# Kernel optimization log

Measured on AMD Instinct MI355X. Metric: run time of the kernel, lower is better.

Reference implementation:

```python
import jax, jax.numpy as jnp
import numpy as np

B, N, C, H = 8, 1024, 768, 12
D = C // H  # head_dim = 64
SCALE = D ** -0.5


def setup_inputs() -> dict:
    key = jax.random.key(0)
    ks = jax.random.split(key, 5)
    s = lambda k, sh, fan: jax.random.normal(k, sh, jnp.float32) * (fan ** -0.5)
    return {
        "x": jax.random.normal(ks[0], (B, N, C), jnp.float32),
        "w_qkv": s(ks[1], (C, 3 * C), C),
        "b_qkv": jnp.zeros((3 * C,), jnp.float32),
        "w_l": s(ks[2], (H, H), H),
        "b_l": jnp.zeros((H,), jnp.float32),
        "w_w": s(ks[3], (H, H), H),
        "b_w": jnp.zeros((H,), jnp.float32),
        "w_proj": s(ks[4], (C, C), C),
        "b_proj": jnp.zeros((C,), jnp.float32),
    }


def reference(x, w_qkv, b_qkv, w_l, b_l, w_w, b_w, w_proj, b_proj):
    Bq, Nq, Cq = x.shape
    # qkv projection -> (3, B, H, N, D)
    qkv = (x @ w_qkv + b_qkv).reshape(Bq, Nq, 3, H, D).transpose(2, 0, 3, 1, 4)
    q, k, v = qkv[0] * SCALE, qkv[1], qkv[2]
    # raw scores [B, H, N, N]
    attn = jnp.einsum("bhnd,bhmd->bhnm", q, k)
    # pre-softmax talking-heads: mix across head axis (Dense over H)
    attn = jnp.einsum("bhnm,hg->bgnm", attn, w_l) + b_l[None, :, None, None]
    attn = jax.nn.softmax(attn, axis=-1)
    # post-softmax talking-heads
    attn = jnp.einsum("bhnm,hg->bgnm", attn, w_w) + b_w[None, :, None, None]
    # weighted values -> (B, N, C)
    out = jnp.einsum("bhnm,bhmd->bnhd", attn, v).reshape(Bq, Nq, Cq)
    return out @ w_proj + b_proj
```

## Files before the change

kernel.cpp:

```cpp
#include <hip/hip_runtime.h>

#define BB 8
#define NN 1024
#define CC 768
#define HH 12
#define DD 64

typedef unsigned short u16;
typedef unsigned int u32;
typedef __attribute__((ext_vector_type(8))) short s16x8;
typedef __attribute__((ext_vector_type(4))) short s16x4;
typedef __attribute__((ext_vector_type(4))) float f32x4;
typedef __attribute__((ext_vector_type(2))) u32 u32x2;
typedef __attribute__((ext_vector_type(4))) u32 u32x4;

__device__ __forceinline__ float bf2f(u16 u) {
  u32 x = ((u32)u) << 16;
  return __builtin_bit_cast(float, x);
}
__device__ __forceinline__ u16 f2bf(float f) {
  u32 x = __builtin_bit_cast(u32, f);
  x += 0x7fffu + ((x >> 16) & 1u);
  return (u16)(x >> 16);
}
__device__ __forceinline__ float hw_exp2(float x) { return __builtin_amdgcn_exp2f(x); }
__device__ __forceinline__ float hw_log2(float x) { return __builtin_amdgcn_logf(x); }
__device__ __forceinline__ s16x8 lds_read8(const u16* p) {
  u32x2 a = *(const u32x2*)p;
  u32x2 b = *(const u32x2*)(p + 4);
  u32x4 m = {a.x, a.y, b.x, b.y};
  return __builtin_bit_cast(s16x8, m);
}
__device__ __forceinline__ u32 packhl(float v) {
  u32 xv = __builtin_bit_cast(u32, v);
  float lo = v - __builtin_bit_cast(float, xv & 0xFFFF0000u);
  return (xv >> 16) | (__builtin_bit_cast(u32, lo) & 0xFFFF0000u);
}
__device__ __forceinline__ void gload_lds16(const u16* g, u16* l) {
  __builtin_amdgcn_global_load_lds(
      (const __attribute__((address_space(1))) u32*)g,
      (__attribute__((address_space(3))) u32*)l, 16, 0, 0);
}

__global__ __launch_bounds__(256) void convx_kernel(const float* __restrict__ in,
                                                    u16* __restrict__ out) {
  size_t i = ((size_t)blockIdx.x * 256 + threadIdx.x) * 8;
  f32x4 a = *(const f32x4*)(in + i);
  f32x4 b = *(const f32x4*)(in + i + 4);
  s16x8 r;
#pragma unroll
  for (int j = 0; j < 4; j++) { r[j] = (short)f2bf(a[j]); r[4 + j] = (short)f2bf(b[j]); }
  *(s16x8*)(out + i) = r;
}

__global__ __launch_bounds__(256) void transpose_kernel(const float* __restrict__ in,
                                                        u16* __restrict__ out,
                                                        int R, int C) {
  __shared__ float t[32][33];
  const int cl = threadIdx.x & 31, rq = threadIdx.x >> 5;
#pragma unroll
  for (int rr = 0; rr < 4; rr++) {
    int rl = rq * 4 + rr;
    t[rl][cl] = in[(size_t)(blockIdx.y * 32 + rl) * C + blockIdx.x * 32 + cl];
  }
  __syncthreads();
#pragma unroll
  for (int rr = 0; rr < 4; rr++) {
    int oc = rq * 4 + rr;
    out[(size_t)(blockIdx.x * 32 + oc) * R + blockIdx.y * 32 + cl] = f2bf(t[cl][oc]);
  }
}

__global__ __launch_bounds__(256) void qkv_gemm(
    const u16* __restrict__ A, const u16* __restrict__ Bt, const float* __restrict__ bias,
    u16* __restrict__ qo, u16* __restrict__ ko, u16* __restrict__ vo) {
  __shared__ __align__(16) u16 As[128 * 32];
  __shared__ __align__(16) u16 Bs[128 * 32];
  const int tid = threadIdx.x;
  const int w = tid >> 6, lane = tid & 63, l15 = lane & 15, l4 = lane >> 4;
  const int wm = w & 1, wn = w >> 1;
  const int m0 = blockIdx.x * 128, n0 = blockIdx.y * 128;
  const int grow = lane >> 2, gcol = (lane & 3) * 8;

  f32x4 acc[4][4];
#pragma unroll
  for (int a = 0; a < 4; a++)
#pragma unroll
    for (int bb = 0; bb < 4; bb++) acc[a][bb] = (f32x4){0.f, 0.f, 0.f, 0.f};

  for (int k0 = 0; k0 < CC; k0 += 32) {
    __syncthreads();
    const u16* ga = A + (size_t)(m0 + w * 32 + grow) * CC + k0 + gcol;
    const u16* gb = Bt + (size_t)(n0 + w * 32 + grow) * CC + k0 + gcol;
    gload_lds16(ga, &As[w * 1024]);
    gload_lds16(ga + (size_t)16 * CC, &As[w * 1024 + 512]);
    gload_lds16(gb, &Bs[w * 1024]);
    gload_lds16(gb + (size_t)16 * CC, &Bs[w * 1024 + 512]);
    __syncthreads();
    s16x8 af[4], bf[4];
#pragma unroll
    for (int a = 0; a < 4; a++) af[a] = *(const s16x8*)&As[(wm * 64 + a * 16 + l15) * 32 + l4 * 8];
#pragma unroll
    for (int bb = 0; bb < 4; bb++) bf[bb] = *(const s16x8*)&Bs[(wn * 64 + bb * 16 + l15) * 32 + l4 * 8];
#pragma unroll
    for (int a = 0; a < 4; a++)
#pragma unroll
      for (int bb = 0; bb < 4; bb++)
        acc[a][bb] = __builtin_amdgcn_mfma_f32_16x16x32_bf16(af[a], bf[bb], acc[a][bb], 0, 0, 0);
  }

  const int b = (m0 >> 10);
#pragma unroll
  for (int bb = 0; bb < 4; bb++) {
    int col = n0 + wn * 64 + bb * 16 + l15;
    int s = col / CC;
    int rem = col - s * CC;
    int h = rem >> 6, d = rem & 63;
    float bv = bias[col];
#pragma unroll
    for (int a = 0; a < 4; a++) {
      int row0 = m0 + wm * 64 + a * 16 + l4 * 4;
      int nt0 = row0 & (NN - 1);
      if (s == 2) {
        s16x4 pk;
#pragma unroll
        for (int r = 0; r < 4; r++) pk[r] = (short)f2bf(acc[a][bb][r] + bv);
        *(s16x4*)(vo + (((size_t)((b * HH + h) * DD + d)) << 10) + nt0) = pk;
      } else if (s == 0) {
#pragma unroll
        for (int r = 0; r < 4; r++)
          qo[(((size_t)((b * HH + h) * NN + nt0 + r)) << 6) + d] = f2bf((acc[a][bb][r] + bv) * 0.125f);
      } else {
#pragma unroll
        for (int r = 0; r < 4; r++)
          ko[(((size_t)((b * HH + h) * NN + nt0 + r)) << 6) + d] = f2bf(acc[a][bb][r] + bv);
      }
    }
  }
}

__global__ __launch_bounds__(256) void proj_gemm(
    const u16* __restrict__ A, const u16* __restrict__ Bt, const float* __restrict__ bias,
    float* __restrict__ out) {
  __shared__ __align__(16) u16 As[128 * 32];
  __shared__ __align__(16) u16 Bs[128 * 32];
  const int tid = threadIdx.x;
  const int w = tid >> 6, lane = tid & 63, l15 = lane & 15, l4 = lane >> 4;
  const int wm = w & 1, wn = w >> 1;
  const int m0 = blockIdx.x * 128, n0 = blockIdx.y * 128;
  const int grow = lane >> 2, gcol = (lane & 3) * 8;

  f32x4 acc[4][4];
#pragma unroll
  for (int a = 0; a < 4; a++)
#pragma unroll
    for (int bb = 0; bb < 4; bb++) acc[a][bb] = (f32x4){0.f, 0.f, 0.f, 0.f};

  for (int k0 = 0; k0 < CC; k0 += 32) {
    __syncthreads();
    const u16* ga = A + (size_t)(m0 + w * 32 + grow) * CC + k0 + gcol;
    const u16* gb = Bt + (size_t)(n0 + w * 32 + grow) * CC + k0 + gcol;
    gload_lds16(ga, &As[w * 1024]);
    gload_lds16(ga + (size_t)16 * CC, &As[w * 1024 + 512]);
    gload_lds16(gb, &Bs[w * 1024]);
    gload_lds16(gb + (size_t)16 * CC, &Bs[w * 1024 + 512]);
    __syncthreads();
    s16x8 af[4], bf[4];
#pragma unroll
    for (int a = 0; a < 4; a++) af[a] = *(const s16x8*)&As[(wm * 64 + a * 16 + l15) * 32 + l4 * 8];
#pragma unroll
    for (int bb = 0; bb < 4; bb++) bf[bb] = *(const s16x8*)&Bs[(wn * 64 + bb * 16 + l15) * 32 + l4 * 8];
#pragma unroll
    for (int a = 0; a < 4; a++)
#pragma unroll
      for (int bb = 0; bb < 4; bb++)
        acc[a][bb] = __builtin_amdgcn_mfma_f32_16x16x32_bf16(af[a], bf[bb], acc[a][bb], 0, 0, 0);
  }

#pragma unroll
  for (int bb = 0; bb < 4; bb++) {
    int col = n0 + wn * 64 + bb * 16 + l15;
    float bv = bias[col];
#pragma unroll
    for (int a = 0; a < 4; a++) {
      int row0 = m0 + wm * 64 + a * 16 + l4 * 4;
#pragma unroll
      for (int r = 0; r < 4; r++)
        out[(size_t)(row0 + r) * CC + col] = acc[a][bb][r] + bv;
    }
  }
}

#define SB_BYTES 28736
#define UT_OFF   SB_BYTES
#define UT_ELE   6912
#define LL2_OFF  (SB_BYTES + 27648)
#define SM_TOTAL (LL2_OFF + 1088)

__global__ __launch_bounds__(512, 4) void attn_kernel(
    const u16* __restrict__ qg, const u16* __restrict__ kg, const u16* __restrict__ vtg,
    const float* __restrict__ wlg, const float* __restrict__ blg,
    const float* __restrict__ wwg, const float* __restrict__ bwg,
    u16* __restrict__ aout) {
  __shared__ __align__(16) char smem[SM_TOTAL];
  u16* Sb = (u16*)smem;
  u16* Ut0 = (u16*)(smem + UT_OFF);
  float* lpart = (float*)(smem + UT_OFF);
  float* ll2 = (float*)(smem + LL2_OFF);

  const int b = blockIdx.x, i0 = blockIdx.y * 16;
  const int tid = threadIdx.x;
  const int w = tid >> 6, lane = tid & 63, l15 = lane & 15, l4 = lane >> 4;
  const float RLN2 = 1.44269504088896340736f;

  for (int j = tid; j < SB_BYTES / 4; j += 512) ((u32*)smem)[j] = 0;
  __syncthreads();

  s16x8 wlS, wlA1, wlA2, wwA1, wwA2;
#pragma unroll
  for (int j = 0; j < 8; j++) {
    int k = l4 * 8 + j;
    float v1 = (k < 12 && l15 < 12) ? wlg[k * 12 + l15] * RLN2 : 0.f;
    wlS[j] = (short)f2bf(v1);
    int h = k >> 1, pt = k & 1;
    float v2 = (h < 12 && l15 < 12) ? wlg[h * 12 + l15] * RLN2 : 0.f;
    u16 h2 = f2bf(v2); u16 lo2 = f2bf(v2 - bf2f(h2));
    wlA1[j] = (short)h2; wlA2[j] = (short)(pt ? 0 : lo2);
    float v3 = (h < 12 && l15 < 12) ? wwg[h * 12 + l15] : 0.f;
    u16 h3 = f2bf(v3); u16 lo3 = f2bf(v3 - bf2f(h3));
    wwA1[j] = (short)h3; wwA2[j] = (short)(pt ? 0 : lo3);
  }
  int gr[4]; float blv[4], bwv[4];
#pragma unroll
  for (int r = 0; r < 4; r++) {
    gr[r] = l4 * 4 + r;
    blv[r] = (gr[r] < 12) ? blg[gr[r]] * RLN2 : 0.f;
    bwv[r] = (gr[r] < 12) ? bwg[gr[r]] : 0.f;
  }

  int jh[3], jmb[3];
  s16x8 qf[3][2];
#pragma unroll
  for (int jt = 0; jt < 3; jt++) {
    int j = w * 3 + jt;
    jh[jt] = j % 12; jmb[jt] = j / 12;
    const u16* qp = qg + (((size_t)((b * HH + jh[jt]) * NN + i0 + l15)) << 6) + l4 * 8;
    qf[jt][0] = *(const s16x8*)qp;
    qf[jt][1] = *(const s16x8*)(qp + 32);
  }

  float la[4] = {0.f, 0.f, 0.f, 0.f};
  for (int mt = 0; mt < 32; mt++) {
    const int m0 = mt * 32;
#pragma unroll
    for (int jt = 0; jt < 3; jt++) {
      f32x4 c = (f32x4){0.f, 0.f, 0.f, 0.f};
      const u16* kp = kg + (((size_t)((b * HH + jh[jt]) * NN + m0 + jmb[jt] * 16 + l15)) << 6) + l4 * 8;
      c = __builtin_amdgcn_mfma_f32_16x16x32_bf16(*(const s16x8*)kp, qf[jt][0], c, 0, 0, 0);
      c = __builtin_amdgcn_mfma_f32_16x16x32_bf16(*(const s16x8*)(kp + 32), qf[jt][1], c, 0, 0, 0);
      int cb = (jmb[jt] * 16 + l4 * 4) * 16 + l15;
#pragma unroll
      for (int r = 0; r < 4; r++)
        Sb[(size_t)(cb + r * 16) * 20 + jh[jt]] = f2bf(c[r]);
    }
    __syncthreads();
#pragma unroll
    for (int tt = 0; tt < 4; tt++) {
      int t = w * 4 + tt;
      s16x8 bS = lds_read8(Sb + (size_t)(t * 16 + l15) * 20 + l4 * 8);
      f32x4 T = (f32x4){blv[0], blv[1], blv[2], blv[3]};
      T = __builtin_amdgcn_mfma_f32_16x16x32_bf16(wlS, bS, T, 0, 0, 0);
#pragma unroll
      for (int r = 0; r < 4; r++) la[r] += hw_exp2(T[r]);
    }
    __syncthreads();
  }

#pragma unroll
  for (int r = 0; r < 4; r++) lpart[w * 256 + gr[r] * 16 + l15] = la[r];
  __syncthreads();
  if (tid < 256) {
    float s = 0.f;
#pragma unroll
    for (int w2 = 0; w2 < 8; w2++) s += lpart[w2 * 256 + tid];
    ll2[(tid >> 4) * 17 + (tid & 15)] = hw_log2(s);
  }
  __syncthreads();
  float Tinit[4];
#pragma unroll
  for (int r = 0; r < 4; r++) Tinit[r] = blv[r] - ll2[gr[r] * 17 + l15];

  const int db = w >> 1, pvh = (w & 1) * 6;
  f32x4 O[6];
#pragma unroll
  for (int jp = 0; jp < 6; jp++) O[jp] = (f32x4){0.f, 0.f, 0.f, 0.f};

  for (int mt = 0; mt < 32; mt++) {
    const int m0 = mt * 32;
    u16* Utb = Ut0 + (mt & 1) * UT_ELE;
#pragma unroll
    for (int jt = 0; jt < 3; jt++) {
      f32x4 c = (f32x4){0.f, 0.f, 0.f, 0.f};
      const u16* kp = kg + (((size_t)((b * HH + jh[jt]) * NN + m0 + jmb[jt] * 16 + l15)) << 6) + l4 * 8;
      c = __builtin_amdgcn_mfma_f32_16x16x32_bf16(*(const s16x8*)kp, qf[jt][0], c, 0, 0, 0);
      c = __builtin_amdgcn_mfma_f32_16x16x32_bf16(*(const s16x8*)(kp + 32), qf[jt][1], c, 0, 0, 0);
      int cb = (jmb[jt] * 16 + l4 * 4) * 16 + l15;
#pragma unroll
      for (int r = 0; r < 4; r++)
        *(u32*)(Sb + (size_t)(cb + r * 16) * 28 + 2 * jh[jt]) = packhl(c[r]);
    }
    __syncthreads();
#pragma unroll
    for (int tt = 0; tt < 4; tt++) {
      int t = w * 4 + tt;
      s16x8 bS = lds_read8(Sb + (size_t)(t * 16 + l15) * 28 + l4 * 8);
      f32x4 T = (f32x4){Tinit[0], Tinit[1], Tinit[2], Tinit[3]};
      T = __builtin_amdgcn_mfma_f32_16x16x32_bf16(wlA1, bS, T, 0, 0, 0);
      T = __builtin_amdgcn_mfma_f32_16x16x32_bf16(wlA2, bS, T, 0, 0, 0);
      u32x4 pk;
#pragma unroll
      for (int r = 0; r < 4; r++) pk[r] = packhl(hw_exp2(T[r]));
      s16x8 bP = __builtin_bit_cast(s16x8, pk);
      f32x4 U = (f32x4){bwv[0], bwv[1], bwv[2], bwv[3]};
      U = __builtin_amdgcn_mfma_f32_16x16x32_bf16(wwA1, bP, U, 0, 0, 0);
      U = __builtin_amdgcn_mfma_f32_16x16x32_bf16(wwA2, bP, U, 0, 0, 0);
#pragma unroll
      for (int r = 0; r < 4; r++)
        if (gr[r] < 12) Utb[(size_t)(gr[r] * 16 + l15) * 36 + t] = f2bf(U[r]);
    }
    __syncthreads();
#pragma unroll
    for (int jp = 0; jp < 6; jp++) {
      const int h = pvh + jp;
      s16x8 aV = *(const s16x8*)(vtg + (((size_t)((b * HH + h) * DD + db * 16 + l15)) << 10) + m0 + l4 * 8);
      s16x8 bU = lds_read8(Utb + (size_t)(h * 16 + l15) * 36 + l4 * 8);
      O[jp] = __builtin_amdgcn_mfma_f32_16x16x32_bf16(aV, bU, O[jp], 0, 0, 0);
    }
  }

#pragma unroll
  for (int jp = 0; jp < 6; jp++) {
    const int h = pvh + jp;
    const int d0 = db * 16 + l4 * 4;
    s16x4 pk4;
#pragma unroll
    for (int r = 0; r < 4; r++) pk4[r] = (short)f2bf(O[jp][r]);
    *(s16x4*)(aout + ((size_t)(b * NN) + i0 + l15) * CC + h * DD + d0) = pk4;
  }
}

extern "C" void kernel_launch(void* const* d_in, const int* in_sizes, int n_in,
                              void* d_out, int out_size, void* d_ws, size_t ws_size,
                              hipStream_t stream) {
  const float* x      = (const float*)d_in[0];
  const float* w_qkv  = (const float*)d_in[1];
  const float* b_qkv  = (const float*)d_in[2];
  const float* w_l    = (const float*)d_in[3];
  const float* b_l    = (const float*)d_in[4];
  const float* w_w    = (const float*)d_in[5];
  const float* b_w    = (const float*)d_in[6];
  const float* w_proj = (const float*)d_in[7];
  const float* b_proj = (const float*)d_in[8];

  const size_t per = (size_t)BB * HH * NN * DD;
  u16* xb  = (u16*)d_ws;
  u16* wqt = xb + per;
  u16* wpt = wqt + (size_t)3 * CC * CC;
  u16* q   = wpt + (size_t)CC * CC;
  u16* k   = q + per;
  u16* vt  = k + per;
  u16* ao  = vt + per;

  convx_kernel<<<3072, 256, 0, stream>>>(x, xb);
  transpose_kernel<<<dim3(3 * CC / 32, CC / 32), 256, 0, stream>>>(w_qkv, wqt, CC, 3 * CC);
  transpose_kernel<<<dim3(CC / 32, CC / 32), 256, 0, stream>>>(w_proj, wpt, CC, CC);
  qkv_gemm<<<dim3(64, 18), 256, 0, stream>>>(xb, wqt, b_qkv, q, k, vt);
  attn_kernel<<<dim3(BB, NN / 16), 512, 0, stream>>>(q, k, vt, w_l, b_l, w_w, b_w, ao);
  proj_gemm<<<dim3(64, 6), 256, 0, stream>>>(ao, wpt, b_proj, (float*)d_out);
}
```

Before: 446.4 us.

## Process 64-key tiles in attention pass one and batch PV loads

The first (log-sum-exp) pass now handles 64 keys per iteration instead of 32. Each warp computes six score tiles over three heads with Q fragments reused across two key blocks, which halves the number of barrier pairs in that pass. The head/key-block mapping changes so each warp owns three consecutive heads in both passes, and only the pass-one score buffer region is zeroed. The PV accumulation is split into two groups of three, with V and U loads issued before the MFMAs to improve latency hiding, at the cost of higher register pressure.

```diff
diff --git a/kernel.cpp b/kernel.cpp
--- a/kernel.cpp
+++ b/kernel.cpp
@@ -194,6 +194,7 @@
 #define SB_BYTES 28736
 #define UT_OFF   SB_BYTES
 #define UT_ELE   6912
+#define P1_ZERO  10272
 #define LL2_OFF  (SB_BYTES + 27648)
 #define SM_TOTAL (LL2_OFF + 1088)
 
@@ -211,9 +212,10 @@
   const int b = blockIdx.x, i0 = blockIdx.y * 16;
   const int tid = threadIdx.x;
   const int w = tid >> 6, lane = tid & 63, l15 = lane & 15, l4 = lane >> 4;
+  const int hg = (w >> 1) * 3;
   const float RLN2 = 1.44269504088896340736f;
 
-  for (int j = tid; j < SB_BYTES / 4; j += 512) ((u32*)smem)[j] = 0;
+  for (int j = tid; j < P1_ZERO; j += 512) ((u32*)smem)[j] = 0;
   __syncthreads();
 
   s16x8 wlS, wlA1, wlA2, wwA1, wwA2;
@@ -238,35 +240,35 @@
     bwv[r] = (gr[r] < 12) ? bwg[gr[r]] : 0.f;
   }
 
-  int jh[3], jmb[3];
   s16x8 qf[3][2];
 #pragma unroll
-  for (int jt = 0; jt < 3; jt++) {
-    int j = w * 3 + jt;
-    jh[jt] = j % 12; jmb[jt] = j / 12;
-    const u16* qp = qg + (((size_t)((b * HH + jh[jt]) * NN + i0 + l15)) << 6) + l4 * 8;
-    qf[jt][0] = *(const s16x8*)qp;
-    qf[jt][1] = *(const s16x8*)(qp + 32);
-  }
-
+  for (int c = 0; c < 3; c++) {
+    const u16* qp = qg + (((size_t)((b * HH + hg + c) * NN + i0 + l15)) << 6) + l4 * 8;
+    qf[c][0] = *(const s16x8*)qp;
+    qf[c][1] = *(const s16x8*)(qp + 32);
+  }
+
+  const int mbase = (w & 1) * 2;
   float la[4] = {0.f, 0.f, 0.f, 0.f};
-  for (int mt = 0; mt < 32; mt++) {
-    const int m0 = mt * 32;
-#pragma unroll
-    for (int jt = 0; jt < 3; jt++) {
-      f32x4 c = (f32x4){0.f, 0.f, 0.f, 0.f};
-      const u16* kp = kg + (((size_t)((b * HH + jh[jt]) * NN + m0 + jmb[jt] * 16 + l15)) << 6) + l4 * 8;
-      c = __builtin_amdgcn_mfma_f32_16x16x32_bf16(*(const s16x8*)kp, qf[jt][0], c, 0, 0, 0);
-      c = __builtin_amdgcn_mfma_f32_16x16x32_bf16(*(const s16x8*)(kp + 32), qf[jt][1], c, 0, 0, 0);
-      int cb = (jmb[jt] * 16 + l4 * 4) * 16 + l15;
+  for (int it = 0; it < 16; it++) {
+    const int m0 = it * 64;
+#pragma unroll
+    for (int jt = 0; jt < 6; jt++) {
+      const int c = jt % 3, mb = mbase + jt / 3;
+      const int h = hg + c;
+      f32x4 s = (f32x4){0.f, 0.f, 0.f, 0.f};
+      const u16* kp = kg + (((size_t)((b * HH + h) * NN + m0 + mb * 16 + l15)) << 6) + l4 * 8;
+      s = __builtin_amdgcn_mfma_f32_16x16x32_bf16(*(const s16x8*)kp, qf[c][0], s, 0, 0, 0);
+      s = __builtin_amdgcn_mfma_f32_16x16x32_bf16(*(const s16x8*)(kp + 32), qf[c][1], s, 0, 0, 0);
+      int cb = (mb * 16 + l4 * 4) * 16 + l15;
 #pragma unroll
       for (int r = 0; r < 4; r++)
-        Sb[(size_t)(cb + r * 16) * 20 + jh[jt]] = f2bf(c[r]);
-    }
-    __syncthreads();
-#pragma unroll
-    for (int tt = 0; tt < 4; tt++) {
-      int t = w * 4 + tt;
+        Sb[(size_t)(cb + r * 16) * 20 + h] = f2bf(s[r]);
+    }
+    __syncthreads();
+#pragma unroll
+    for (int tt = 0; tt < 8; tt++) {
+      int t = w * 8 + tt;
       s16x8 bS = lds_read8(Sb + (size_t)(t * 16 + l15) * 20 + l4 * 8);
       f32x4 T = (f32x4){blv[0], blv[1], blv[2], blv[3]};
       T = __builtin_amdgcn_mfma_f32_16x16x32_bf16(wlS, bS, T, 0, 0, 0);
@@ -291,6 +293,7 @@
   for (int r = 0; r < 4; r++) Tinit[r] = blv[r] - ll2[gr[r] * 17 + l15];
 
   const int db = w >> 1, pvh = (w & 1) * 6;
+  const int mb2 = w & 1;
   f32x4 O[6];
 #pragma unroll
   for (int jp = 0; jp < 6; jp++) O[jp] = (f32x4){0.f, 0.f, 0.f, 0.f};
@@ -300,14 +303,15 @@
     u16* Utb = Ut0 + (mt & 1) * UT_ELE;
 #pragma unroll
     for (int jt = 0; jt < 3; jt++) {
+      const int h = hg + jt;
       f32x4 c = (f32x4){0.f, 0.f, 0.f, 0.f};
-      const u16* kp = kg + (((size_t)((b * HH + jh[jt]) * NN + m0 + jmb[jt] * 16 + l15)) << 6) + l4 * 8;
+      const u16* kp = kg + (((size_t)((b * HH + h) * NN + m0 + mb2 * 16 + l15)) << 6) + l4 * 8;
       c = __builtin_amdgcn_mfma_f32_16x16x32_bf16(*(const s16x8*)kp, qf[jt][0], c, 0, 0, 0);
       c = __builtin_amdgcn_mfma_f32_16x16x32_bf16(*(const s16x8*)(kp + 32), qf[jt][1], c, 0, 0, 0);
-      int cb = (jmb[jt] * 16 + l4 * 4) * 16 + l15;
+      int cb = (mb2 * 16 + l4 * 4) * 16 + l15;
 #pragma unroll
       for (int r = 0; r < 4; r++)
-        *(u32*)(Sb + (size_t)(cb + r * 16) * 28 + 2 * jh[jt]) = packhl(c[r]);
+        *(u32*)(Sb + (size_t)(cb + r * 16) * 28 + 2 * h) = packhl(c[r]);
     }
     __syncthreads();
 #pragma unroll
@@ -329,12 +333,29 @@
         if (gr[r] < 12) Utb[(size_t)(gr[r] * 16 + l15) * 36 + t] = f2bf(U[r]);
     }
     __syncthreads();
-#pragma unroll
-    for (int jp = 0; jp < 6; jp++) {
-      const int h = pvh + jp;
-      s16x8 aV = *(const s16x8*)(vtg + (((size_t)((b * HH + h) * DD + db * 16 + l15)) << 10) + m0 + l4 * 8);
-      s16x8 bU = lds_read8(Utb + (size_t)(h * 16 + l15) * 36 + l4 * 8);
-      O[jp] = __builtin_amdgcn_mfma_f32_16x16x32_bf16(aV, bU, O[jp], 0, 0, 0);
+    {
+      const u16* vb = vtg + (((size_t)((b * HH + pvh) * DD + db * 16 + l15)) << 10) + m0 + l4 * 8;
+      const size_t vstep = (size_t)DD << 10;
+      const u16* ub = Utb + (size_t)(pvh * 16 + l15) * 36 + l4 * 8;
+      const size_t ustep = (size_t)16 * 36;
+      s16x8 aV0 = *(const s16x8*)vb;
+      s16x8 aV1 = *(const s16x8*)(vb + vstep);
+      s16x8 aV2 = *(const s16x8*)(vb + 2 * vstep);
+      s16x8 bU0 = lds_read8(ub);
+      s16x8 bU1 = lds_read8(ub + ustep);
+      s16x8 bU2 = lds_read8(ub + 2 * ustep);
+      O[0] = __builtin_amdgcn_mfma_f32_16x16x32_bf16(aV0, bU0, O[0], 0, 0, 0);
+      O[1] = __builtin_amdgcn_mfma_f32_16x16x32_bf16(aV1, bU1, O[1], 0, 0, 0);
+      O[2] = __builtin_amdgcn_mfma_f32_16x16x32_bf16(aV2, bU2, O[2], 0, 0, 0);
+      s16x8 aV3 = *(const s16x8*)(vb + 3 * vstep);
+      s16x8 aV4 = *(const s16x8*)(vb + 4 * vstep);
+      s16x8 aV5 = *(const s16x8*)(vb + 5 * vstep);
+      s16x8 bU3 = lds_read8(ub + 3 * ustep);
+      s16x8 bU4 = lds_read8(ub + 4 * ustep);
+      s16x8 bU5 = lds_read8(ub + 5 * ustep);
+      O[3] = __builtin_amdgcn_mfma_f32_16x16x32_bf16(aV3, bU3, O[3], 0, 0, 0);
+      O[4] = __builtin_amdgcn_mfma_f32_16x16x32_bf16(aV4, bU4, O[4], 0, 0, 0);
+      O[5] = __builtin_amdgcn_mfma_f32_16x16x32_bf16(aV5, bU5, O[5], 0, 0, 0);
     }
   }
 
```

Result: slower. 471.7 us (+5.7%).
